# Optimization experiments

Hardware: AMD Instinct MI355X
Metric: run time of the kernel (lower is better)

The kernel has to match this reference:

```python
import jax, jax.numpy as jnp
import numpy as np

N = 100000   # nodes
DEG = 16     # kNN degree
D = 32       # feature dim
E = N * DEG  # edges


def setup_inputs() -> dict:
    key = jax.random.key(0)
    k1, k2 = jax.random.split(key)
    x = jax.random.normal(k1, (N, D), dtype=jnp.float32)
    indptr = jnp.arange(N + 1, dtype=jnp.int32) * DEG  # uniform-degree CSR
    indices = jax.random.randint(k2, (E,), 0, N, dtype=jnp.int32)
    return {"input": x, "indptr": indptr, "indices": indices}


def reference(input, indptr, indices):
    # CSR segment max: out[i] = max_{e in [indptr[i], indptr[i+1])} input[indices[e]]
    n_nodes = indptr.shape[0] - 1
    counts = jnp.diff(indptr)
    seg_ids = jnp.repeat(
        jnp.arange(n_nodes, dtype=jnp.int32), counts,
        total_repeat_length=indices.shape[0])
    gathered = input[indices]  # [E, D] irregular gather
    out = jax.ops.segment_max(gathered, seg_ids, num_segments=n_nodes)
    return out
```

## Files before the change

### kernel.cpp

```cpp
#include <hip/hip_runtime.h>
#include <math.h>


typedef float fv4 __attribute__((ext_vector_type(4)));

#define LANES_PER_NODE 8
#define NODES_PER_BLOCK 32

static __device__ __forceinline__ fv4 fmax4(fv4 a, fv4 b) {
    fv4 r;
    r.x = fmaxf(a.x, b.x);
    r.y = fmaxf(a.y, b.y);
    r.z = fmaxf(a.z, b.z);
    r.w = fmaxf(a.w, b.w);
    return r;
}

__global__ __launch_bounds__(256) void seg_max_kernel(
    const float* __restrict__ x,
    const int* __restrict__ indptr,
    const int* __restrict__ indices,
    float* __restrict__ out,
    int n_nodes,
    int n_edges)
{
    const int c    = threadIdx.x & (LANES_PER_NODE - 1);
    const int node = blockIdx.x * NODES_PER_BLOCK + (threadIdx.x >> 3);
    if (node >= n_nodes) return;

    const fv4* __restrict__ x4 = reinterpret_cast<const fv4*>(x);

    fv4 acc = { -INFINITY, -INFINITY, -INFINITY, -INFINITY };

    const bool spec_ok = ((long long)node * 16 + 16 <= (long long)n_edges);

    if (spec_ok) {
        const int4* __restrict__ idx4 =
            reinterpret_cast<const int4*>(indices) + node * 4;
        const int4 i0 = idx4[0];
        const int4 i1 = idx4[1];
        const int4 i2 = idx4[2];
        const int4 i3 = idx4[3];

        const int start = indptr[node];
        const int end   = indptr[node + 1];

        if (start == node * 16 && end == start + 16) {
            const fv4 v0  = x4[i0.x * LANES_PER_NODE + c];
            const fv4 v1  = x4[i0.y * LANES_PER_NODE + c];
            const fv4 v2  = x4[i0.z * LANES_PER_NODE + c];
            const fv4 v3  = x4[i0.w * LANES_PER_NODE + c];
            const fv4 v4  = x4[i1.x * LANES_PER_NODE + c];
            const fv4 v5  = x4[i1.y * LANES_PER_NODE + c];
            const fv4 v6  = x4[i1.z * LANES_PER_NODE + c];
            const fv4 v7  = x4[i1.w * LANES_PER_NODE + c];
            const fv4 v8  = x4[i2.x * LANES_PER_NODE + c];
            const fv4 v9  = x4[i2.y * LANES_PER_NODE + c];
            const fv4 v10 = x4[i2.z * LANES_PER_NODE + c];
            const fv4 v11 = x4[i2.w * LANES_PER_NODE + c];
            const fv4 v12 = x4[i3.x * LANES_PER_NODE + c];
            const fv4 v13 = x4[i3.y * LANES_PER_NODE + c];
            const fv4 v14 = x4[i3.z * LANES_PER_NODE + c];
            const fv4 v15 = x4[i3.w * LANES_PER_NODE + c];

            fv4 a0 = fmax4(v0,  v1);
            fv4 a1 = fmax4(v2,  v3);
            fv4 a2 = fmax4(v4,  v5);
            fv4 a3 = fmax4(v6,  v7);
            fv4 a4 = fmax4(v8,  v9);
            fv4 a5 = fmax4(v10, v11);
            fv4 a6 = fmax4(v12, v13);
            fv4 a7 = fmax4(v14, v15);
            fv4 b0 = fmax4(a0, a1);
            fv4 b1 = fmax4(a2, a3);
            fv4 b2 = fmax4(a4, a5);
            fv4 b3 = fmax4(a6, a7);
            acc = fmax4(fmax4(b0, b1), fmax4(b2, b3));
        } else {
            for (int e = start; e < end; ++e) {
                const int row = indices[e];
                acc = fmax4(acc, x4[row * LANES_PER_NODE + c]);
            }
        }
    } else {
        const int start = indptr[node];
        const int end   = indptr[node + 1];
        for (int e = start; e < end; ++e) {
            const int row = indices[e];
            acc = fmax4(acc, x4[row * LANES_PER_NODE + c]);
        }
    }

    __builtin_nontemporal_store(
        acc, reinterpret_cast<fv4*>(out) + node * LANES_PER_NODE + c);
}

extern "C" void kernel_launch(void* const* d_in, const int* in_sizes, int n_in,
                              void* d_out, int out_size, void* d_ws, size_t ws_size,
                              hipStream_t stream) {
    const float* x       = (const float*)d_in[0];
    const int*   indptr  = (const int*)d_in[1];
    const int*   indices = (const int*)d_in[2];
    float*       out     = (float*)d_out;

    const int n_nodes = in_sizes[1] - 1;
    const int n_edges = in_sizes[2];

    const int grid = (n_nodes + NODES_PER_BLOCK - 1) / NODES_PER_BLOCK;
    seg_max_kernel<<<grid, 256, 0, stream>>>(x, indptr, indices, out,
                                             n_nodes, n_edges);
}
```

Baseline: 91.47 us.

## Slice neighbor gather by source row range for cache locality

The fixed-degree fast path now sweeps over eight contiguous ranges of source rows. Each neighbor's load is issued only during the pass whose range contains its row, with four independent accumulators. The goal is to concentrate the set of rows being gathered at any moment so they stay resident in L2. In exchange it adds eight rounds of compare-and-branch per lane and serialises loads, which lowers memory-level parallelism.

```diff
diff --git a/kernel.cpp b/kernel.cpp
--- a/kernel.cpp
+++ b/kernel.cpp
@@ -6,6 +6,7 @@
 
 #define LANES_PER_NODE 8
 #define NODES_PER_BLOCK 32
+#define NSLICES 8
 
 static __device__ __forceinline__ fv4 fmax4(fv4 a, fv4 b) {
     fv4 r;
@@ -22,7 +23,8 @@
     const int* __restrict__ indices,
     float* __restrict__ out,
     int n_nodes,
-    int n_edges)
+    int n_edges,
+    int slice_w)
 {
     const int c    = threadIdx.x & (LANES_PER_NODE - 1);
     const int node = blockIdx.x * NODES_PER_BLOCK + (threadIdx.x >> 3);
@@ -30,10 +32,12 @@
 
     const fv4* __restrict__ x4 = reinterpret_cast<const fv4*>(x);
 
-    fv4 acc = { -INFINITY, -INFINITY, -INFINITY, -INFINITY };
+    fv4 acc0 = { -INFINITY, -INFINITY, -INFINITY, -INFINITY };
+    fv4 acc1 = acc0, acc2 = acc0, acc3 = acc0;
 
     const bool spec_ok = ((long long)node * 16 + 16 <= (long long)n_edges);
 
+    bool fast = false;
     if (spec_ok) {
         const int4* __restrict__ idx4 =
             reinterpret_cast<const int4*>(indices) + node * 4;
@@ -44,52 +48,53 @@
 
         const int start = indptr[node];
         const int end   = indptr[node + 1];
+        fast = (start == node * 16) && (end == start + 16);
 
-        if (start == node * 16 && end == start + 16) {
-            const fv4 v0  = x4[i0.x * LANES_PER_NODE + c];
-            const fv4 v1  = x4[i0.y * LANES_PER_NODE + c];
-            const fv4 v2  = x4[i0.z * LANES_PER_NODE + c];
-            const fv4 v3  = x4[i0.w * LANES_PER_NODE + c];
-            const fv4 v4  = x4[i1.x * LANES_PER_NODE + c];
-            const fv4 v5  = x4[i1.y * LANES_PER_NODE + c];
-            const fv4 v6  = x4[i1.z * LANES_PER_NODE + c];
-            const fv4 v7  = x4[i1.w * LANES_PER_NODE + c];
-            const fv4 v8  = x4[i2.x * LANES_PER_NODE + c];
-            const fv4 v9  = x4[i2.y * LANES_PER_NODE + c];
-            const fv4 v10 = x4[i2.z * LANES_PER_NODE + c];
-            const fv4 v11 = x4[i2.w * LANES_PER_NODE + c];
-            const fv4 v12 = x4[i3.x * LANES_PER_NODE + c];
-            const fv4 v13 = x4[i3.y * LANES_PER_NODE + c];
-            const fv4 v14 = x4[i3.z * LANES_PER_NODE + c];
-            const fv4 v15 = x4[i3.w * LANES_PER_NODE + c];
+        if (fast) {
+            const int r0 = i0.x, r1 = i0.y, r2  = i0.z, r3  = i0.w;
+            const int r4 = i1.x, r5 = i1.y, r6  = i1.z, r7  = i1.w;
+            const int r8 = i2.x, r9 = i2.y, r10 = i2.z, r11 = i2.w;
+            const int r12 = i3.x, r13 = i3.y, r14 = i3.z, r15 = i3.w;
 
-            fv4 a0 = fmax4(v0,  v1);
-            fv4 a1 = fmax4(v2,  v3);
-            fv4 a2 = fmax4(v4,  v5);
-            fv4 a3 = fmax4(v6,  v7);
-            fv4 a4 = fmax4(v8,  v9);
-            fv4 a5 = fmax4(v10, v11);
-            fv4 a6 = fmax4(v12, v13);
-            fv4 a7 = fmax4(v14, v15);
-            fv4 b0 = fmax4(a0, a1);
-            fv4 b1 = fmax4(a2, a3);
-            fv4 b2 = fmax4(a4, a5);
-            fv4 b3 = fmax4(a6, a7);
-            acc = fmax4(fmax4(b0, b1), fmax4(b2, b3));
-        } else {
-            for (int e = start; e < end; ++e) {
-                const int row = indices[e];
-                acc = fmax4(acc, x4[row * LANES_PER_NODE + c]);
+#define GATHER_IF(r, A) \
+            if ((r) >= lo && (r) < hi) \
+                A = fmax4(A, x4[(r) * LANES_PER_NODE + c]);
+
+            #pragma unroll
+            for (int s = 0; s < NSLICES; ++s) {
+                const int lo = s * slice_w;
+                const int hi = lo + slice_w;
+                GATHER_IF(r0,  acc0)
+                GATHER_IF(r1,  acc1)
+                GATHER_IF(r2,  acc2)
+                GATHER_IF(r3,  acc3)
+                GATHER_IF(r4,  acc0)
+                GATHER_IF(r5,  acc1)
+                GATHER_IF(r6,  acc2)
+                GATHER_IF(r7,  acc3)
+                GATHER_IF(r8,  acc0)
+                GATHER_IF(r9,  acc1)
+                GATHER_IF(r10, acc2)
+                GATHER_IF(r11, acc3)
+                GATHER_IF(r12, acc0)
+                GATHER_IF(r13, acc1)
+                GATHER_IF(r14, acc2)
+                GATHER_IF(r15, acc3)
             }
+#undef GATHER_IF
         }
-    } else {
+    }
+
+    if (!fast) {
         const int start = indptr[node];
         const int end   = indptr[node + 1];
         for (int e = start; e < end; ++e) {
             const int row = indices[e];
-            acc = fmax4(acc, x4[row * LANES_PER_NODE + c]);
+            acc0 = fmax4(acc0, x4[row * LANES_PER_NODE + c]);
         }
     }
+
+    const fv4 acc = fmax4(fmax4(acc0, acc1), fmax4(acc2, acc3));
 
     __builtin_nontemporal_store(
         acc, reinterpret_cast<fv4*>(out) + node * LANES_PER_NODE + c);
@@ -105,8 +110,10 @@
 
     const int n_nodes = in_sizes[1] - 1;
     const int n_edges = in_sizes[2];
+    const int n_rows  = in_sizes[0] / 32;
+    const int slice_w = (n_rows + NSLICES - 1) / NSLICES;
 
     const int grid = (n_nodes + NODES_PER_BLOCK - 1) / NODES_PER_BLOCK;
     seg_max_kernel<<<grid, 256, 0, stream>>>(x, indptr, indices, out,
-                                             n_nodes, n_edges);
+                                             n_nodes, n_edges, slice_w);
 }
```

After: 134.5 us. +47.0%, slower.
